# Performance work log

Measured on AMD Instinct MI355X. Metric: run time of the kernel, lower is better.

Reference implementation:

```python
import jax, jax.numpy as jnp
import numpy as np

D_MODEL = 2048
NUM_HEADS = 16
D_K = D_MODEL // NUM_HEADS
THETA = 10000.0
BATCH, SEQ = 2, 2048


def setup_inputs() -> dict:
    key = jax.random.key(0)
    ks = jax.random.split(key, 5)
    scale = 1.0 / np.sqrt(D_MODEL)
    x = jax.random.normal(ks[0], (BATCH, SEQ, D_MODEL), dtype=jnp.float32)
    token_positions = jnp.broadcast_to(jnp.arange(SEQ, dtype=jnp.int32)[None, :], (BATCH, SEQ))
    Wq = jax.random.normal(ks[1], (D_MODEL, D_MODEL), dtype=jnp.float32) * scale
    Wk = jax.random.normal(ks[2], (D_MODEL, D_MODEL), dtype=jnp.float32) * scale
    Wv = jax.random.normal(ks[3], (D_MODEL, D_MODEL), dtype=jnp.float32) * scale
    Wo = jax.random.normal(ks[4], (D_MODEL, D_MODEL), dtype=jnp.float32) * scale
    return {"x": x, "token_positions": token_positions, "Wq": Wq, "Wk": Wk, "Wv": Wv, "Wo": Wo}


def _apply_rope(t, positions):
    # t: [b, h, s, d_k]; positions: [b, s]. Interleaved-pair rotation.
    half = D_K // 2
    inv_freq = THETA ** (-jnp.arange(0, half, dtype=jnp.float32) * 2.0 / D_K)  # [half]
    ang = positions.astype(jnp.float32)[:, :, None] * inv_freq[None, None, :]  # [b, s, half]
    cos = jnp.cos(ang)[:, None, :, :]  # [b, 1, s, half]
    sin = jnp.sin(ang)[:, None, :, :]
    t2 = t.reshape(*t.shape[:-1], half, 2)
    x1, x2 = t2[..., 0], t2[..., 1]
    r1 = x1 * cos - x2 * sin
    r2 = x1 * sin + x2 * cos
    return jnp.stack([r1, r2], axis=-1).reshape(t.shape)


def reference(x, token_positions, Wq, Wk, Wv, Wo):
    b, s, _ = x.shape
    # Linear layers compute x @ W^T (weight stored as [out, in], no bias)
    def proj(w):
        y = jnp.einsum('bsd,ed->bse', x, w)
        return y.reshape(b, s, NUM_HEADS, D_K).transpose(0, 2, 1, 3)  # b h s d
    Q, K, V = proj(Wq), proj(Wk), proj(Wv)
    Q = _apply_rope(Q, token_positions)
    K = _apply_rope(K, token_positions)
    scores = jnp.einsum('bhqd,bhkd->bhqk', Q, K) / jnp.sqrt(jnp.float32(D_K))
    causal = jnp.tril(jnp.ones((s, s), dtype=bool))
    scores = jnp.where(causal[None, None], scores, jnp.finfo(scores.dtype).min)
    attn = jax.nn.softmax(scores, axis=-1)
    out = jnp.einsum('bhqk,bhkd->bhqd', attn, V)  # b h s d
    out = out.transpose(0, 2, 1, 3).reshape(b, s, D_MODEL)
    return jnp.einsum('bse,de->bsd', out, Wo)
```

## Files before the change

kernel.cpp:

```cpp
#include <hip/hip_runtime.h>
#include <cstdint>
#include <cstddef>

#define D_MODEL 2048
#define NHEAD 16
#define DK 128
#define SEQ 2048
#define BATCH 2
#define NTOK (BATCH * SEQ)
#define NQB 32

typedef __bf16 bf16;
typedef __bf16 bf16x2 __attribute__((ext_vector_type(2)));
typedef __bf16 bf16x4 __attribute__((ext_vector_type(4)));
typedef __bf16 bf16x8 __attribute__((ext_vector_type(8)));
typedef float f32x4 __attribute__((ext_vector_type(4)));

__device__ __forceinline__ void g2lds16(const void* g, void* l) {
  __builtin_amdgcn_global_load_lds(
      (const __attribute__((address_space(1))) void*)g,
      (__attribute__((address_space(3))) void*)l, 16, 0, 0);
}

__device__ __forceinline__ void cstore(float* p, float v) { *p = v; }
__device__ __forceinline__ void cstore(bf16* p, float v) { *p = (bf16)v; }

#define BAR()                              \
  {                                        \
    asm volatile("" ::: "memory");         \
    __builtin_amdgcn_s_barrier();          \
    asm volatile("" ::: "memory");         \
  }

__global__ void k_conv5(const float* __restrict__ X, const float* __restrict__ W0,
                        const float* __restrict__ W1, const float* __restrict__ W2,
                        const float* __restrict__ W3, bf16* __restrict__ xo,
                        bf16* __restrict__ o0, bf16* __restrict__ o1,
                        bf16* __restrict__ o2, bf16* __restrict__ o3,
                        int nx4, int nw4) {
  const float* in;
  bf16* out;
  int n;
  switch (blockIdx.y) {
    case 0: in = X; out = xo; n = nx4; break;
    case 1: in = W0; out = o0; n = nw4; break;
    case 2: in = W1; out = o1; n = nw4; break;
    case 3: in = W2; out = o2; n = nw4; break;
    default: in = W3; out = o3; n = nw4;
  }
  int i = blockIdx.x * blockDim.x + threadIdx.x;
  if (i >= n) return;
  const float4 v = ((const float4*)in)[i];
  bf16x4 o = {(bf16)v.x, (bf16)v.y, (bf16)v.z, (bf16)v.w};
  ((bf16x4*)out)[i] = o;
}

__global__ __launch_bounds__(512, 1) void k_qkv(
    const bf16* __restrict__ xb, const bf16* __restrict__ wq,
    const bf16* __restrict__ wk, const bf16* __restrict__ wv,
    bf16* __restrict__ Qb, bf16* __restrict__ Kb, bf16* __restrict__ VTg,
    const int* __restrict__ pos) {
  __shared__ bf16 smem[65536];

  const int wg = blockIdx.x;
  const int t = threadIdx.x;
  const int wid = t >> 6, lane = t & 63;
  const int lr = lane & 15, lg = lane >> 4;
  const int srow = wid * 8 + (lane >> 3);
  const int schunk = ((lane & 7) ^ ((lane >> 3) & 7)) * 8;
  const int K = D_MODEL;
  const int T = K >> 6;

  if (wg < 256) {
    const int z = wg >> 7;
    const int i = wg & 127;
    const int bn = i & 7, bm = i >> 3;
    const bf16* Bp = z ? wk : wq;
    bf16* Cp = z ? Kb : Qb;
    const int wr = wid >> 2, wc = wid & 3;
    const size_t arow0 = (size_t)bm * 256;
    const size_t brow0 = (size_t)bn * 256;
    bf16* AbB = smem;
    bf16* BbB = smem + 32768;

#define QSTG(X, row0, k0, lb, h)                                               \
  {                                                                            \
    g2lds16(&(X)[((row0) + (h)*128 + srow) * (size_t)K + (k0) + schunk],       \
            &(lb)[((h)*128 + wid * 8) * 64]);                                  \
    g2lds16(&(X)[((row0) + (h)*128 + 64 + srow) * (size_t)K + (k0) + schunk],  \
            &(lb)[((h)*128 + 64 + wid * 8) * 64]);                             \
  }
#define QLDA(lb, mh, m, kk) \
  (*(const bf16x8*)&(lb)[((mh)*128 + wr * 64 + (m)*16 + lr) * 64 + ((((kk)*4 + lg) ^ (lr & 7)) * 8)])
#define QLDB(lb, nh, n, kk) \
  (*(const bf16x8*)&(lb)[((nh)*128 + wc * 32 + (n)*16 + lr) * 64 + ((((kk)*4 + lg) ^ (lr & 7)) * 8)])

    QSTG(xb, arow0, 0, (AbB + 0), 0);
    QSTG(xb, arow0, 0, (AbB + 0), 1);
    QSTG(Bp, brow0, 0, (BbB + 0), 0);
    QSTG(Bp, brow0, 0, (BbB + 0), 1);
    QSTG(xb, arow0, 64, (AbB + 16384), 0);

    f32x4 acc[2][2][4][2] = {};

    for (int tt = 0; tt < T; ++tt) {
      const int cur = tt & 1;
      const bf16* Ac = AbB + cur * 16384;
      const bf16* Bc = BbB + cur * 16384;
      bf16* Aw = AbB + cur * 16384;
      bf16* An = AbB + (cur ^ 1) * 16384;
      bf16* Bn = BbB + (cur ^ 1) * 16384;
      const int k1 = (tt + 1) << 6;
      const int k2 = (tt + 2) << 6;
      const bool pf1 = (tt + 1 < T);
      const bool pf2 = (tt + 2 < T);

      if (tt == T - 1) {
        asm volatile("s_waitcnt vmcnt(0)" ::: "memory");
      } else {
        asm volatile("s_waitcnt vmcnt(2)" ::: "memory");
      }
      BAR();

      bf16x8 a[4][2], b0[2][2], b1[2][2];

#pragma unroll
      for (int m = 0; m < 4; ++m)
#pragma unroll
        for (int kk = 0; kk < 2; ++kk) a[m][kk] = QLDA(Ac, 0, m, kk);
#pragma unroll
      for (int n = 0; n < 2; ++n)
#pragma unroll
        for (int kk = 0; kk < 2; ++kk) b0[n][kk] = QLDB(Bc, 0, n, kk);
      if (pf1) {
        QSTG(xb, arow0, k1, An, 1);
        QSTG(Bp, brow0, k1, Bn, 0);
      }
      __builtin_amdgcn_s_setprio(1);
#pragma unroll
      for (int m = 0; m < 4; ++m)
#pragma unroll
        for (int n = 0; n < 2; ++n)
#pragma unroll
          for (int kk = 0; kk < 2; ++kk)
            acc[0][0][m][n] =
                __builtin_amdgcn_mfma_f32_16x16x32_bf16(a[m][kk], b0[n][kk], acc[0][0][m][n], 0, 0, 0);
      __builtin_amdgcn_s_setprio(0);
      BAR();

#pragma unroll
      for (int n = 0; n < 2; ++n)
#pragma unroll
        for (int kk = 0; kk < 2; ++kk) b1[n][kk] = QLDB(Bc, 1, n, kk);
      if (pf1) QSTG(Bp, brow0, k1, Bn, 1);
      __builtin_amdgcn_s_setprio(1);
#pragma unroll
      for (int m = 0; m < 4; ++m)
#pragma unroll
        for (int n = 0; n < 2; ++n)
#pragma unroll
          for (int kk = 0; kk < 2; ++kk)
            acc[0][1][m][n] =
                __builtin_amdgcn_mfma_f32_16x16x32_bf16(a[m][kk], b1[n][kk], acc[0][1][m][n], 0, 0, 0);
      __builtin_amdgcn_s_setprio(0);

#pragma unroll
      for (int m = 0; m < 4; ++m)
#pragma unroll
        for (int kk = 0; kk < 2; ++kk) a[m][kk] = QLDA(Ac, 1, m, kk);
      if (pf2) QSTG(xb, arow0, k2, Aw, 0);
      __builtin_amdgcn_s_setprio(1);
#pragma unroll
      for (int m = 0; m < 4; ++m)
#pragma unroll
        for (int n = 0; n < 2; ++n)
#pragma unroll
          for (int kk = 0; kk < 2; ++kk)
            acc[1][1][m][n] =
                __builtin_amdgcn_mfma_f32_16x16x32_bf16(a[m][kk], b1[n][kk], acc[1][1][m][n], 0, 0, 0);

#pragma unroll
      for (int m = 0; m < 4; ++m)
#pragma unroll
        for (int n = 0; n < 2; ++n)
#pragma unroll
          for (int kk = 0; kk < 2; ++kk)
            acc[1][0][m][n] =
                __builtin_amdgcn_mfma_f32_16x16x32_bf16(a[m][kk], b0[n][kk], acc[1][0][m][n], 0, 0, 0);
      __builtin_amdgcn_s_setprio(0);
    }

    float invf[2];
#pragma unroll
    for (int n = 0; n < 2; ++n) {
      int f = ((wc * 32 + n * 16 + lr) & 127) >> 1;
      invf[n] = exp2f((float)f * -0.20762050593121503f);
    }
#pragma unroll
    for (int mh = 0; mh < 2; ++mh)
#pragma unroll
      for (int m = 0; m < 4; ++m) {
        size_t rowb = arow0 + mh * 128 + wr * 64 + m * 16 + lg * 4;
#pragma unroll
        for (int r = 0; r < 4; ++r) {
          float p = (float)pos[rowb + r];
#pragma unroll
          for (int n = 0; n < 2; ++n) {
            float sn, cs;
            __sincosf(p * invf[n], &sn, &cs);
#pragma unroll
            for (int nh = 0; nh < 2; ++nh) {
              float v = acc[mh][nh][m][n][r];
              float vp = __shfl_xor(v, 1);
              float outv = (lr & 1) ? (v * cs + vp * sn) : (v * cs - vp * sn);
              size_t col = brow0 + nh * 128 + wc * 32 + n * 16 + lr;
              Cp[(rowb + r) * D_MODEL + col] = (bf16)outv;
            }
          }
        }
      }
#undef QSTG
#undef QLDA
#undef QLDB
  } else {
    const int u = wg - 256;
    const int batch = u >> 7;
    const int i = u & 127;
    const int bn = i & 7, bm = i >> 3;
    const size_t boff = (size_t)batch * 2048 * 2048;
    const bf16* Bp = xb + boff;
    bf16* Cp = VTg + boff;
    const int wr = wid >> 2, wc = wid & 3;
    const size_t arow0 = (size_t)bm * 128;
    const size_t brow0 = (size_t)bn * 256;
    bf16* AbB = smem;
    bf16* BbB = smem + 16384;

#define VSTGA(X, k0, lb, h) \
  g2lds16(&(X)[(arow0 + (h)*64 + srow) * (size_t)K + (k0) + schunk], &(lb)[((h)*64 + wid * 8) * 64]);
#define VSTGB(X, k0, lb, h)                                                       \
  {                                                                               \
    g2lds16(&(X)[(brow0 + (h)*128 + srow) * (size_t)K + (k0) + schunk],           \
            &(lb)[((h)*128 + wid * 8) * 64]);                                     \
    g2lds16(&(X)[(brow0 + (h)*128 + 64 + srow) * (size_t)K + (k0) + schunk],      \
            &(lb)[((h)*128 + 64 + wid * 8) * 64]);                                \
  }
#define VLDA(lb, mh, m, kk) \
  (*(const bf16x8*)&(lb)[((mh)*64 + wr * 32 + (m)*16 + lr) * 64 + ((((kk)*4 + lg) ^ (lr & 7)) * 8)])
#define VLDB(lb, nh, n, kk) \
  (*(const bf16x8*)&(lb)[((nh)*128 + wc * 32 + (n)*16 + lr) * 64 + ((((kk)*4 + lg) ^ (lr & 7)) * 8)])

    VSTGA(wv, 0, (AbB + 0), 0);
    VSTGA(wv, 0, (AbB + 0), 1);
    VSTGB(Bp, 0, (BbB + 0), 0);
    VSTGB(Bp, 0, (BbB + 0), 1);
    VSTGA(wv, 64, (AbB + 8192), 0);

    f32x4 acc[2][2][2][2] = {};

    for (int tt = 0; tt < T; ++tt) {
      const int cur = tt & 1;
      const bf16* Ac = AbB + cur * 8192;
      const bf16* Bc = BbB + cur * 16384;
      bf16* Aw = AbB + cur * 8192;
      bf16* An = AbB + (cur ^ 1) * 8192;
      bf16* Bn = BbB + (cur ^ 1) * 16384;
      const int k1 = (tt + 1) << 6;
      const int k2 = (tt + 2) << 6;
      const bool pf1 = (tt + 1 < T);
      const bool pf2 = (tt + 2 < T);

      if (tt == T - 1) {
        asm volatile("s_waitcnt vmcnt(0)" ::: "memory");
      } else {
        asm volatile("s_waitcnt vmcnt(1)" ::: "memory");
      }
      BAR();

      bf16x8 a[2][2], b[2][2];

#pragma unroll
      for (int m = 0; m < 2; ++m)
#pragma unroll
        for (int kk = 0; kk < 2; ++kk) a[m][kk] = VLDA(Ac, 0, m, kk);
#pragma unroll
      for (int n = 0; n < 2; ++n)
#pragma unroll
        for (int kk = 0; kk < 2; ++kk) b[n][kk] = VLDB(Bc, 0, n, kk);
      if (pf1) {
        VSTGA(wv, k1, An, 1);
        VSTGB(Bp, k1, Bn, 0);
      }
      __builtin_amdgcn_s_setprio(1);
#pragma unroll
      for (int m = 0; m < 2; ++m)
#pragma unroll
        for (int n = 0; n < 2; ++n)
#pragma unroll
          for (int kk = 0; kk < 2; ++kk)
            acc[0][0][m][n] =
                __builtin_amdgcn_mfma_f32_16x16x32_bf16(a[m][kk], b[n][kk], acc[0][0][m][n], 0, 0, 0);
      __builtin_amdgcn_s_setprio(0);
      BAR();

#pragma unroll
      for (int n = 0; n < 2; ++n)
#pragma unroll
        for (int kk = 0; kk < 2; ++kk) b[n][kk] = VLDB(Bc, 1, n, kk);
      if (pf1) VSTGB(Bp, k1, Bn, 1);
      __builtin_amdgcn_s_setprio(1);
#pragma unroll
      for (int m = 0; m < 2; ++m)
#pragma unroll
        for (int n = 0; n < 2; ++n)
#pragma unroll
          for (int kk = 0; kk < 2; ++kk)
            acc[0][1][m][n] =
                __builtin_amdgcn_mfma_f32_16x16x32_bf16(a[m][kk], b[n][kk], acc[0][1][m][n], 0, 0, 0);
      __builtin_amdgcn_s_setprio(0);
      BAR();

#pragma unroll
      for (int m = 0; m < 2; ++m)
#pragma unroll
        for (int kk = 0; kk < 2; ++kk) a[m][kk] = VLDA(Ac, 1, m, kk);
      if (pf2) VSTGA(wv, k2, Aw, 0);
      __builtin_amdgcn_s_setprio(1);
#pragma unroll
      for (int m = 0; m < 2; ++m)
#pragma unroll
        for (int n = 0; n < 2; ++n)
#pragma unroll
          for (int kk = 0; kk < 2; ++kk)
            acc[1][1][m][n] =
                __builtin_amdgcn_mfma_f32_16x16x32_bf16(a[m][kk], b[n][kk], acc[1][1][m][n], 0, 0, 0);
      __builtin_amdgcn_s_setprio(0);
      BAR();

#pragma unroll
      for (int n = 0; n < 2; ++n)
#pragma unroll
        for (int kk = 0; kk < 2; ++kk) b[n][kk] = VLDB(Bc, 0, n, kk);
      __builtin_amdgcn_s_setprio(1);
#pragma unroll
      for (int m = 0; m < 2; ++m)
#pragma unroll
        for (int n = 0; n < 2; ++n)
#pragma unroll
          for (int kk = 0; kk < 2; ++kk)
            acc[1][0][m][n] =
                __builtin_amdgcn_mfma_f32_16x16x32_bf16(a[m][kk], b[n][kk], acc[1][0][m][n], 0, 0, 0);
      __builtin_amdgcn_s_setprio(0);
    }

#pragma unroll
    for (int mh = 0; mh < 2; ++mh)
#pragma unroll
      for (int nh = 0; nh < 2; ++nh)
#pragma unroll
        for (int m = 0; m < 2; ++m) {
          size_t rowb = arow0 + mh * 64 + wr * 32 + m * 16 + lg * 4;
#pragma unroll
          for (int n = 0; n < 2; ++n) {
            size_t col = brow0 + nh * 128 + wc * 32 + n * 16 + lr;
#pragma unroll
            for (int r = 0; r < 4; ++r) Cp[(rowb + r) * SEQ + col] = (bf16)acc[mh][nh][m][n][r];
          }
        }
#undef VSTGA
#undef VSTGB
#undef VLDA
#undef VLDB
  }
}

template <typename OutT>
__global__ __launch_bounds__(256, 2) void k_gemm_nt(
    const bf16* __restrict__ A, const bf16* __restrict__ B0, const bf16* __restrict__ B1,
    const bf16* __restrict__ B2, OutT* __restrict__ C0, OutT* __restrict__ C1,
    OutT* __restrict__ C2, int M, int N, int K) {
  const bf16* Bp = B0;
  OutT* Cp = C0;
  if (blockIdx.z == 1) { Bp = B1; Cp = C1; }
  else if (blockIdx.z == 2) { Bp = B2; Cp = C2; }

  __shared__ bf16 As[128 * 32];
  __shared__ bf16 Bs[128 * 32];

  const int t = threadIdx.x;
  const int w = t >> 6;
  const int lane = t & 63;
  const int lr = lane & 15;
  const int lg = lane >> 4;
  const int wr = w >> 1, wc = w & 1;
  const int bm = blockIdx.y, bn = blockIdx.x;

  f32x4 acc[4][4] = {};

  const int srow = lane >> 2;
  const int scol = (lane & 3) * 8;

  const int kt_iters = K >> 5;
  for (int kt = 0; kt < kt_iters; ++kt) {
    const int kbase = kt * 32;
#pragma unroll
    for (int i = 0; i < 2; ++i) {
      int chunk = w * 2 + i;
      int row = chunk * 16 + srow;
      g2lds16(&A[(size_t)(bm * 128 + row) * K + kbase + scol], &As[chunk * 512]);
      g2lds16(&Bp[(size_t)(bn * 128 + row) * K + kbase + scol], &Bs[chunk * 512]);
    }
    asm volatile("s_waitcnt vmcnt(0)" ::: "memory");
    __syncthreads();

    bf16x8 af[4], bfr[4];
#pragma unroll
    for (int m = 0; m < 4; ++m)
      af[m] = *(const bf16x8*)&As[(wr * 64 + m * 16 + lr) * 32 + lg * 8];
#pragma unroll
    for (int n = 0; n < 4; ++n)
      bfr[n] = *(const bf16x8*)&Bs[(wc * 64 + n * 16 + lr) * 32 + lg * 8];
#pragma unroll
    for (int m = 0; m < 4; ++m)
#pragma unroll
      for (int n = 0; n < 4; ++n)
        acc[m][n] = __builtin_amdgcn_mfma_f32_16x16x32_bf16(af[m], bfr[n], acc[m][n], 0, 0, 0);
    __syncthreads();
  }

#pragma unroll
  for (int m = 0; m < 4; ++m) {
    int rowb = bm * 128 + wr * 64 + m * 16 + lg * 4;
#pragma unroll
    for (int n = 0; n < 4; ++n) {
      int col = bn * 128 + wc * 64 + n * 16 + lr;
#pragma unroll
      for (int r = 0; r < 4; ++r) cstore(&Cp[(size_t)(rowb + r) * N + col], acc[m][n][r]);
    }
  }
}

__global__ __launch_bounds__(256, 2) void k_attn(const bf16* __restrict__ Q,
                                                 const bf16* __restrict__ K,
                                                 const bf16* __restrict__ VT,
                                                 bf16* __restrict__ O) {
  const int wg = blockIdx.x;
  const int g = wg & 7;
  const int i = wg >> 3;
  const int bh = g + 8 * (i & 3);
  const int pr = i >> 2;
  const int b = bh >> 4, h = bh & 15;

  const int t = threadIdx.x;
  const int w = t >> 6, lane = t & 63;
  const int lr = lane & 15, lg = lane >> 4;

  const size_t rowbase = (size_t)b * SEQ;
  const int hoff = h * DK;
  const size_t vtbase = (size_t)bh * DK * SEQ;

  __shared__ bf16 Ks[2][64 * 128];
  __shared__ bf16 VTb[2][128 * 64];
  __shared__ bf16 Pb[4][16 * 64];

  const float scale2 = 0.12751744672f;
  const float FIXM2 = 11.5415603271f;

  int cur = 0;

  const int krow_l = lane >> 4;
  const int kchunk = lane & 15;
  const int vrow_l = lane >> 3;
  const int vchunk = lane & 7;

  for (int qsel = 0; qsel < 2; ++qsel) {
    const int qblk = qsel ? pr : (NQB - 1 - pr);
    const int qb = qblk * 64;
    const int ktiles = qblk + 1;

    bf16x8 qf[4];
    {
      size_t qrow = rowbase + qb + w * 16 + lr;
#pragma unroll
      for (int c = 0; c < 4; ++c)
        qf[c] = *(const bf16x8*)&Q[qrow * D_MODEL + hoff + c * 32 + lg * 8];
    }

    f32x4 o[8] = {};
    f32x4 lrow = {};

    const bf16* kst[4];
    const bf16* vst[4];
#pragma unroll
    for (int j = 0; j < 4; ++j) {
      int row_ = w * 16 + j * 4 + krow_l;
      kst[j] = &K[(rowbase + row_) * D_MODEL + hoff + (kchunk ^ (row_ & 15)) * 8];
      int d_ = w * 32 + j * 8 + vrow_l;
      vst[j] = &VT[vtbase + (size_t)d_ * SEQ + (vchunk ^ (d_ & 7)) * 8];
    }

#pragma unroll
    for (int j = 0; j < 4; ++j) {
      g2lds16(kst[j], &Ks[cur][(size_t)(w * 16 + j * 4) * 128]);
      kst[j] += 64 * D_MODEL;
    }
#pragma unroll
    for (int j = 0; j < 4; ++j) {
      g2lds16(vst[j], &VTb[cur][(size_t)(w * 32 + j * 8) * 64]);
      vst[j] += 64;
    }

    for (int kt = 0; kt < ktiles; ++kt) {
      const int k0 = kt * 64;
      asm volatile("s_waitcnt vmcnt(0)" ::: "memory");
      __syncthreads();

      if (kt + 1 < ktiles) {
#pragma unroll
        for (int j = 0; j < 4; ++j) {
          g2lds16(kst[j], &Ks[cur ^ 1][(size_t)(w * 16 + j * 4) * 128]);
          kst[j] += 64 * D_MODEL;
        }
#pragma unroll
        for (int j = 0; j < 4; ++j) {
          g2lds16(vst[j], &VTb[cur ^ 1][(size_t)(w * 32 + j * 8) * 64]);
          vst[j] += 64;
        }
      }

      f32x4 sc[4];
      __builtin_amdgcn_s_setprio(1);
#pragma unroll
      for (int tt = 0; tt < 4; ++tt) {
        f32x4 a = {};
#pragma unroll
        for (int c = 0; c < 4; ++c) {
          bf16x8 kf = *(const bf16x8*)&Ks[cur][(tt * 16 + lr) * 128 + (((c * 4 + lg) ^ lr) * 8)];
          a = __builtin_amdgcn_mfma_f32_16x16x32_bf16(qf[c], kf, a, 0, 0, 0);
        }
        sc[tt] = a * scale2;
      }
      __builtin_amdgcn_s_setprio(0);

      const int qrow0 = qb + w * 16 + lg * 4;
      if (k0 + 64 > qb + w * 16) {
#pragma unroll
        for (int tt = 0; tt < 4; ++tt) {
          int kcol = k0 + tt * 16 + lr;
#pragma unroll
          for (int r = 0; r < 4; ++r)
            if (kcol > qrow0 + r) sc[tt][r] = -3.0e38f;
        }
      }

#pragma unroll
      for (int tt = 0; tt < 4; ++tt)
#pragma unroll
        for (int r = 0; r < 4; ++r) {
          float p = __builtin_amdgcn_exp2f(sc[tt][r] - FIXM2);
          sc[tt][r] = p;
          lrow[r] += p;
        }

#pragma unroll
      for (int tt = 0; tt < 4; ++tt)
#pragma unroll
        for (int r = 0; r < 4; ++r) {
          int q = lg * 4 + r;
          int col = tt * 16 + lr;
          Pb[w][q * 64 + (col ^ ((q & 7) << 3))] = (bf16)sc[tt][r];
        }
      asm volatile("s_waitcnt lgkmcnt(0)" ::: "memory");
      bf16x8 pf0 = *(const bf16x8*)&Pb[w][lr * 64 + ((lg * 8) ^ ((lr & 7) << 3))];
      bf16x8 pf1 = *(const bf16x8*)&Pb[w][lr * 64 + ((32 + lg * 8) ^ ((lr & 7) << 3))];

      __builtin_amdgcn_s_setprio(1);
#pragma unroll
      for (int nt = 0; nt < 8; ++nt) {
        int d = nt * 16 + lr;
        bf16x8 vf0 = *(const bf16x8*)&VTb[cur][d * 64 + ((lg ^ (d & 7)) * 8)];
        bf16x8 vf1 = *(const bf16x8*)&VTb[cur][d * 64 + (((4 + lg) ^ (d & 7)) * 8)];
        o[nt] = __builtin_amdgcn_mfma_f32_16x16x32_bf16(pf0, vf0, o[nt], 0, 0, 0);
        o[nt] = __builtin_amdgcn_mfma_f32_16x16x32_bf16(pf1, vf1, o[nt], 0, 0, 0);
      }
      __builtin_amdgcn_s_setprio(0);
      cur ^= 1;
    }

#pragma unroll
    for (int off = 8; off >= 1; off >>= 1)
#pragma unroll
      for (int r = 0; r < 4; ++r) lrow[r] += __shfl_xor(lrow[r], off);

    size_t orow = rowbase + qb + w * 16 + lg * 4;
#pragma unroll
    for (int nt = 0; nt < 8; ++nt)
#pragma unroll
      for (int r = 0; r < 4; ++r)
        O[(orow + r) * D_MODEL + hoff + nt * 16 + lr] = (bf16)(o[nt][r] / lrow[r]);
  }
}

extern "C" void kernel_launch(void* const* d_in, const int* in_sizes, int n_in, void* d_out,
                              int out_size, void* d_ws, size_t ws_size, hipStream_t stream) {
  const float* x = (const float*)d_in[0];
  const int* pos = (const int*)d_in[1];
  const float* Wq = (const float*)d_in[2];
  const float* Wk = (const float*)d_in[3];
  const float* Wv = (const float*)d_in[4];
  const float* Wo = (const float*)d_in[5];
  float* out = (float*)d_out;

  char* ws = (char*)d_ws;
  const size_t MB = 1u << 20;
  bf16* xb  = (bf16*)(ws);
  bf16* wqb = (bf16*)(ws + 16 * MB);
  bf16* wkb = (bf16*)(ws + 24 * MB);
  bf16* wvb = (bf16*)(ws + 32 * MB);
  bf16* wob = (bf16*)(ws + 40 * MB);
  bf16* Qb  = (bf16*)(ws + 48 * MB);
  bf16* Kb  = (bf16*)(ws + 64 * MB);
  bf16* VTg = (bf16*)(ws + 80 * MB);
  bf16* AOb = (bf16*)(ws + 96 * MB);

  {
    int nx4 = NTOK * D_MODEL / 4;
    int nw4 = D_MODEL * D_MODEL / 4;
    k_conv5<<<dim3((nx4 + 255) / 256, 5), 256, 0, stream>>>(
        x, Wq, Wk, Wv, Wo, xb, wqb, wkb, wvb, wob, nx4, nw4);
  }
  k_qkv<<<512, 512, 0, stream>>>(xb, wqb, wkb, wvb, Qb, Kb, VTg, pos);
  k_attn<<<dim3(NQB * NHEAD * BATCH / 2, 1, 1), 256, 0, stream>>>(Qb, Kb, VTg, AOb);
  {
    dim3 g(D_MODEL / 128, NTOK / 128, 1);
    k_gemm_nt<float><<<g, 256, 0, stream>>>(AOb, wob, wob, wob, out, out, out, NTOK, D_MODEL, D_MODEL);
  }
}
```

Before: 229.8 us.

## Rewrite output projection GEMM with larger tiles, double buffering and swizzled LDS

Replaces the simple 128x128, K=32 single-buffered output projection GEMM with a 128x256-tile, 512-thread kernel. It uses K=64 double-buffered LDS with an XOR swizzle and staggers global-to-LDS prefetches across four MFMA phases, with priority hints around the MFMA blocks. The goal is to hide load latency, avoid LDS bank conflicts and increase data reuse per tile. In exchange it launches only 256 workgroups at one block per CU and needs more LDS and registers.

New measurement: 227.9 us. No clear change (-0.8%).

```diff
diff --git a/kernel.cpp b/kernel.cpp
--- a/kernel.cpp
+++ b/kernel.cpp
@@ -375,69 +375,163 @@
 }
 
 template <typename OutT>
-__global__ __launch_bounds__(256, 2) void k_gemm_nt(
-    const bf16* __restrict__ A, const bf16* __restrict__ B0, const bf16* __restrict__ B1,
-    const bf16* __restrict__ B2, OutT* __restrict__ C0, OutT* __restrict__ C1,
-    OutT* __restrict__ C2, int M, int N, int K) {
-  const bf16* Bp = B0;
-  OutT* Cp = C0;
-  if (blockIdx.z == 1) { Bp = B1; Cp = C1; }
-  else if (blockIdx.z == 2) { Bp = B2; Cp = C2; }
-
-  __shared__ bf16 As[128 * 32];
-  __shared__ bf16 Bs[128 * 32];
+__global__ __launch_bounds__(512, 1) void k_gemmW(
+    const bf16* __restrict__ A, const bf16* __restrict__ Bw, OutT* __restrict__ C,
+    int M, int N, int K) {
+  const int wg = blockIdx.x;
+  const int bn = wg & 7;
+  const int bm = wg >> 3;
+
+  __shared__ bf16 Ab[2][128 * 64];
+  __shared__ bf16 Bb[2][256 * 64];
 
   const int t = threadIdx.x;
-  const int w = t >> 6;
-  const int lane = t & 63;
-  const int lr = lane & 15;
-  const int lg = lane >> 4;
-  const int wr = w >> 1, wc = w & 1;
-  const int bm = blockIdx.y, bn = blockIdx.x;
-
-  f32x4 acc[4][4] = {};
-
-  const int srow = lane >> 2;
-  const int scol = (lane & 3) * 8;
-
-  const int kt_iters = K >> 5;
-  for (int kt = 0; kt < kt_iters; ++kt) {
-    const int kbase = kt * 32;
-#pragma unroll
-    for (int i = 0; i < 2; ++i) {
-      int chunk = w * 2 + i;
-      int row = chunk * 16 + srow;
-      g2lds16(&A[(size_t)(bm * 128 + row) * K + kbase + scol], &As[chunk * 512]);
-      g2lds16(&Bp[(size_t)(bn * 128 + row) * K + kbase + scol], &Bs[chunk * 512]);
-    }
-    asm volatile("s_waitcnt vmcnt(0)" ::: "memory");
-    __syncthreads();
-
-    bf16x8 af[4], bfr[4];
-#pragma unroll
-    for (int m = 0; m < 4; ++m)
-      af[m] = *(const bf16x8*)&As[(wr * 64 + m * 16 + lr) * 32 + lg * 8];
-#pragma unroll
-    for (int n = 0; n < 4; ++n)
-      bfr[n] = *(const bf16x8*)&Bs[(wc * 64 + n * 16 + lr) * 32 + lg * 8];
-#pragma unroll
-    for (int m = 0; m < 4; ++m)
-#pragma unroll
-      for (int n = 0; n < 4; ++n)
-        acc[m][n] = __builtin_amdgcn_mfma_f32_16x16x32_bf16(af[m], bfr[n], acc[m][n], 0, 0, 0);
-    __syncthreads();
-  }
-
-#pragma unroll
-  for (int m = 0; m < 4; ++m) {
-    int rowb = bm * 128 + wr * 64 + m * 16 + lg * 4;
-#pragma unroll
-    for (int n = 0; n < 4; ++n) {
-      int col = bn * 128 + wc * 64 + n * 16 + lr;
-#pragma unroll
-      for (int r = 0; r < 4; ++r) cstore(&Cp[(size_t)(rowb + r) * N + col], acc[m][n][r]);
-    }
-  }
+  const int wid = t >> 6, lane = t & 63;
+  const int wr = wid >> 2, wc = wid & 3;
+  const int lr = lane & 15, lg = lane >> 4;
+  const size_t arow0 = (size_t)bm * 128;
+  const size_t brow0 = (size_t)bn * 256;
+
+  const int srow = wid * 8 + (lane >> 3);
+  const int schunk = ((lane & 7) ^ ((lane >> 3) & 7)) * 8;
+
+#define WSTGA(X, k0, lb, h) \
+  g2lds16(&(X)[(arow0 + (h)*64 + srow) * (size_t)K + (k0) + schunk], &(lb)[((h)*64 + wid * 8) * 64]);
+#define WSTGB(X, k0, lb, h)                                                       \
+  {                                                                               \
+    g2lds16(&(X)[(brow0 + (h)*128 + srow) * (size_t)K + (k0) + schunk],           \
+            &(lb)[((h)*128 + wid * 8) * 64]);                                     \
+    g2lds16(&(X)[(brow0 + (h)*128 + 64 + srow) * (size_t)K + (k0) + schunk],      \
+            &(lb)[((h)*128 + 64 + wid * 8) * 64]);                                \
+  }
+#define WLDA(lb, mh, m, kk) \
+  (*(const bf16x8*)&(lb)[((mh)*64 + wr * 32 + (m)*16 + lr) * 64 + ((((kk)*4 + lg) ^ (lr & 7)) * 8)])
+#define WLDB(lb, nh, n, kk) \
+  (*(const bf16x8*)&(lb)[((nh)*128 + wc * 32 + (n)*16 + lr) * 64 + ((((kk)*4 + lg) ^ (lr & 7)) * 8)])
+
+  const int T = K >> 6;
+
+  WSTGA(A, 0, Ab[0], 0);
+  WSTGA(A, 0, Ab[0], 1);
+  WSTGB(Bw, 0, Bb[0], 0);
+  WSTGB(Bw, 0, Bb[0], 1);
+  WSTGA(A, 64, Ab[1], 0);
+
+  f32x4 acc[2][2][2][2] = {};
+
+  for (int tt = 0; tt < T; ++tt) {
+    const int cur = tt & 1;
+    const bf16* Ac = Ab[cur];
+    const bf16* Bc = Bb[cur];
+    bf16* Aw = Ab[cur];
+    bf16* An = Ab[cur ^ 1];
+    bf16* Bn = Bb[cur ^ 1];
+    const int k1 = (tt + 1) << 6;
+    const int k2 = (tt + 2) << 6;
+    const bool pf1 = (tt + 1 < T);
+    const bool pf2 = (tt + 2 < T);
+
+    if (tt == T - 1) {
+      asm volatile("s_waitcnt vmcnt(0)" ::: "memory");
+    } else {
+      asm volatile("s_waitcnt vmcnt(1)" ::: "memory");
+    }
+    BAR();
+
+    bf16x8 a[2][2], b[2][2];
+
+#pragma unroll
+    for (int m = 0; m < 2; ++m)
+#pragma unroll
+      for (int kk = 0; kk < 2; ++kk) a[m][kk] = WLDA(Ac, 0, m, kk);
+#pragma unroll
+    for (int n = 0; n < 2; ++n)
+#pragma unroll
+      for (int kk = 0; kk < 2; ++kk) b[n][kk] = WLDB(Bc, 0, n, kk);
+    if (pf1) {
+      WSTGA(A, k1, An, 1);
+      WSTGB(Bw, k1, Bn, 0);
+    }
+    __builtin_amdgcn_s_setprio(1);
+#pragma unroll
+    for (int m = 0; m < 2; ++m)
+#pragma unroll
+      for (int n = 0; n < 2; ++n)
+#pragma unroll
+        for (int kk = 0; kk < 2; ++kk)
+          acc[0][0][m][n] =
+              __builtin_amdgcn_mfma_f32_16x16x32_bf16(a[m][kk], b[n][kk], acc[0][0][m][n], 0, 0, 0);
+    __builtin_amdgcn_s_setprio(0);
+    BAR();
+
+#pragma unroll
+    for (int n = 0; n < 2; ++n)
+#pragma unroll
+      for (int kk = 0; kk < 2; ++kk) b[n][kk] = WLDB(Bc, 1, n, kk);
+    if (pf1) WSTGB(Bw, k1, Bn, 1);
+    __builtin_amdgcn_s_setprio(1);
+#pragma unroll
+    for (int m = 0; m < 2; ++m)
+#pragma unroll
+      for (int n = 0; n < 2; ++n)
+#pragma unroll
+        for (int kk = 0; kk < 2; ++kk)
+          acc[0][1][m][n] =
+              __builtin_amdgcn_mfma_f32_16x16x32_bf16(a[m][kk], b[n][kk], acc[0][1][m][n], 0, 0, 0);
+    __builtin_amdgcn_s_setprio(0);
+    BAR();
+
+#pragma unroll
+    for (int m = 0; m < 2; ++m)
+#pragma unroll
+      for (int kk = 0; kk < 2; ++kk) a[m][kk] = WLDA(Ac, 1, m, kk);
+    if (pf2) WSTGA(A, k2, Aw, 0);
+    __builtin_amdgcn_s_setprio(1);
+#pragma unroll
+    for (int m = 0; m < 2; ++m)
+#pragma unroll
+      for (int n = 0; n < 2; ++n)
+#pragma unroll
+        for (int kk = 0; kk < 2; ++kk)
+          acc[1][1][m][n] =
+              __builtin_amdgcn_mfma_f32_16x16x32_bf16(a[m][kk], b[n][kk], acc[1][1][m][n], 0, 0, 0);
+    __builtin_amdgcn_s_setprio(0);
+    BAR();
+
+#pragma unroll
+    for (int n = 0; n < 2; ++n)
+#pragma unroll
+      for (int kk = 0; kk < 2; ++kk) b[n][kk] = WLDB(Bc, 0, n, kk);
+    __builtin_amdgcn_s_setprio(1);
+#pragma unroll
+    for (int m = 0; m < 2; ++m)
+#pragma unroll
+      for (int n = 0; n < 2; ++n)
+#pragma unroll
+        for (int kk = 0; kk < 2; ++kk)
+          acc[1][0][m][n] =
+              __builtin_amdgcn_mfma_f32_16x16x32_bf16(a[m][kk], b[n][kk], acc[1][0][m][n], 0, 0, 0);
+    __builtin_amdgcn_s_setprio(0);
+  }
+
+#pragma unroll
+  for (int mh = 0; mh < 2; ++mh)
+#pragma unroll
+    for (int nh = 0; nh < 2; ++nh)
+#pragma unroll
+      for (int m = 0; m < 2; ++m) {
+        size_t rowb = arow0 + mh * 64 + wr * 32 + m * 16 + lg * 4;
+#pragma unroll
+        for (int n = 0; n < 2; ++n) {
+          size_t col = brow0 + nh * 128 + wc * 32 + n * 16 + lr;
+#pragma unroll
+          for (int r = 0; r < 4; ++r) cstore(&C[(rowb + r) * N + col], acc[mh][nh][m][n][r]);
+        }
+      }
+#undef WSTGA
+#undef WSTGB
+#undef WLDA
+#undef WLDB
 }
 
 __global__ __launch_bounds__(256, 2) void k_attn(const bf16* __restrict__ Q,
@@ -631,8 +725,5 @@
   }
   k_qkv<<<512, 512, 0, stream>>>(xb, wqb, wkb, wvb, Qb, Kb, VTg, pos);
   k_attn<<<dim3(NQB * NHEAD * BATCH / 2, 1, 1), 256, 0, stream>>>(Qb, Kb, VTg, AOb);
-  {
-    dim3 g(D_MODEL / 128, NTOK / 128, 1);
-    k_gemm_nt<float><<<g, 256, 0, stream>>>(AOb, wob, wob, wob, out, out, out, NTOK, D_MODEL, D_MODEL);
-  }
+  k_gemmW<float><<<256, 512, 0, stream>>>(AOb, wob, out, NTOK, D_MODEL, D_MODEL);
 }
```
